# Optimization experiments

Measured on AMD Instinct MI355X. Metric: run time of the kernel, lower is better.

Reference implementation:

```python
import jax, jax.numpy as jnp
import numpy as np

N = 32768          # tokens
D_IN = 1024        # input_dim
H = 512            # hidden_dim
K = 4096           # codebook_size
NC = 3             # num_codebooks


def setup_inputs() -> dict:
    key = jax.random.key(0)
    ks = jax.random.split(key, 7)
    s = 0.02  # small init for linear weights
    return {
        "x": jax.random.normal(ks[0], (N, D_IN), dtype=jnp.float32),
        "enc_w1": jax.random.normal(ks[1], (D_IN, 2 * H), dtype=jnp.float32) * s,
        "enc_b1": jnp.zeros((2 * H,), dtype=jnp.float32),
        "enc_w2": jax.random.normal(ks[2], (2 * H, H), dtype=jnp.float32) * s,
        "enc_b2": jnp.zeros((H,), dtype=jnp.float32),
        "dec_w1": jax.random.normal(ks[3], (H, 2 * H), dtype=jnp.float32) * s,
        "dec_b1": jnp.zeros((2 * H,), dtype=jnp.float32),
        "dec_w2": jax.random.normal(ks[4], (2 * H, D_IN), dtype=jnp.float32) * s,
        "dec_b2": jnp.zeros((D_IN,), dtype=jnp.float32),
        "codebooks": jax.random.normal(ks[5], (NC, K, H), dtype=jnp.float32),
    }


def reference(x, enc_w1, enc_b1, enc_w2, enc_b2,
              dec_w1, dec_b1, dec_w2, dec_b2, codebooks):
    # encoder MLP: [N, D_IN] -> [N, H]
    h = jax.nn.relu(x @ enc_w1 + enc_b1) @ enc_w2 + enc_b2

    residual = h
    quantized = jnp.zeros_like(h)
    indices = []
    for i in range(NC):  # fixed small number of codebook stages
        cb = codebooks[i]  # [K, H]
        # squared Euclidean distances (argmin-equivalent to torch.cdist)
        d = (jnp.sum(residual * residual, axis=1, keepdims=True)
             - 2.0 * residual @ cb.T
             + jnp.sum(cb * cb, axis=1))  # [N, K]
        idx = jnp.argmin(d, axis=1)       # [N]
        sel = cb[idx]                     # gather [N, H]
        indices.append(idx)
        quantized = quantized + sel
        residual = residual - sel

    # decoder MLP: [N, H] -> [N, D_IN]
    reconstructed = jax.nn.relu(quantized @ dec_w1 + dec_b1) @ dec_w2 + dec_b2
    # eval-mode forward: loss is None in the original; omit it here
    return quantized, jnp.stack(indices), reconstructed
```

## Files before the change

kernel.cpp:

```cpp
#include <hip/hip_runtime.h>

#define N_TOK 32768
#define DIN   1024
#define HID   512
#define H2    1024
#define KCB   4096
#define NCB   3
#define CHUNK_E 4096
#define CHUNK_D 8192
#define MARGIN 0.25f

typedef _Float16 f16x8 __attribute__((ext_vector_type(8)));
typedef float f32x4 __attribute__((ext_vector_type(4)));
typedef unsigned short u16;

__device__ inline u16 f2h_bits(float v) {
  union { _Float16 f; u16 u; } cv;
  cv.f = (_Float16)v;
  return cv.u;
}
__device__ inline float h_bits2f(u16 u) {
  union { _Float16 f; u16 u; } cv;
  cv.u = u;
  return (float)cv.f;
}
__device__ inline void fsplit(float v, u16& hi, u16& lo) {
  _Float16 h = (_Float16)v;
  float hf = (float)h;
  union { _Float16 f; u16 u; } ch; ch.f = h; hi = ch.u;
  lo = f2h_bits((v - hf) * 2048.0f);
}

#define SWZ(r) (((r) >> 1) & 3)

__device__ inline void stage16(const u16* gplane, int growbase, int lrowbase,
                               int k0, u16* ldsbase, int l, int stride) {
  const int rp = l >> 2, s = l & 3;
  const int sp = s ^ SWZ(lrowbase + rp);
  const u16* src = gplane + (size_t)(growbase + rp) * stride + k0 + sp * 8;
  __builtin_amdgcn_global_load_lds(
      (const __attribute__((address_space(1))) void*)src,
      (__attribute__((address_space(3))) void*)ldsbase, 16, 0, 0);
}

template <bool RELU, bool SPLIT>
__global__ __launch_bounds__(256) void gemm_f32ek(
    const float* __restrict__ A, const float* __restrict__ B,
    const float* __restrict__ bias, float* __restrict__ C,
    u16* __restrict__ Chi, u16* __restrict__ Clo,
    int M, int K, int Nn) {
  __shared__ float As[16][68];
  __shared__ float Bs[16][68];
  const int tid = threadIdx.x;
  const int tx = tid & 15, ty = tid >> 4;
  const int tx4 = tx * 4, ty4 = ty * 4;
  const int m0 = blockIdx.y * 64, n0 = blockIdx.x * 64;

  const int ar = tid >> 2;
  const int aq = (tid & 3) * 4;
  const int bk = tid >> 4;
  const int bn = (tid & 15) * 4;

  float acc[4][4] = {};

  for (int k0 = 0; k0 < K; k0 += 16) {
    float4 av = *(const float4*)(A + (size_t)(m0 + ar) * K + k0 + aq);
    As[aq + 0][ar] = av.x; As[aq + 1][ar] = av.y;
    As[aq + 2][ar] = av.z; As[aq + 3][ar] = av.w;
    *(float4*)(&Bs[bk][bn]) = *(const float4*)(B + (size_t)(k0 + bk) * Nn + n0 + bn);
    __syncthreads();
#pragma unroll
    for (int kk = 0; kk < 16; ++kk) {
      float4 a4 = *(float4*)(&As[kk][ty4]);
      float4 b4 = *(float4*)(&Bs[kk][tx4]);
      float a[4] = {a4.x, a4.y, a4.z, a4.w};
      float bv[4] = {b4.x, b4.y, b4.z, b4.w};
#pragma unroll
      for (int i = 0; i < 4; ++i)
#pragma unroll
        for (int j = 0; j < 4; ++j) acc[i][j] = fmaf(a[i], bv[j], acc[i][j]);
    }
    __syncthreads();
  }

  float bb[4];
#pragma unroll
  for (int j = 0; j < 4; ++j) bb[j] = bias[n0 + tx4 + j];
#pragma unroll
  for (int i = 0; i < 4; ++i) {
    const size_t row = (size_t)(m0 + ty4 + i);
    if (SPLIT) {
      ushort4 h4, l4;
      u16 hs[4], ls[4];
#pragma unroll
      for (int j = 0; j < 4; ++j) {
        float v = acc[i][j] + bb[j];
        if (RELU) v = v > 0.0f ? v : 0.0f;
        fsplit(v, hs[j], ls[j]);
      }
      h4.x = hs[0]; h4.y = hs[1]; h4.z = hs[2]; h4.w = hs[3];
      l4.x = ls[0]; l4.y = ls[1]; l4.z = ls[2]; l4.w = ls[3];
      *(ushort4*)(&Chi[row * Nn + n0 + tx4]) = h4;
      *(ushort4*)(&Clo[row * Nn + n0 + tx4]) = l4;
    } else {
      float4 o;
      float vv[4];
#pragma unroll
      for (int j = 0; j < 4; ++j) {
        float v = acc[i][j] + bb[j];
        if (RELU) v = v > 0.0f ? v : 0.0f;
        vv[j] = v;
      }
      o.x = vv[0]; o.y = vv[1]; o.z = vv[2]; o.w = vv[3];
      *(float4*)(&C[row * Nn + n0 + tx4]) = o;
    }
  }
}

template <bool RELU, bool F16OUT>
__global__ __launch_bounds__(256) void gemm_mfma_f16(
    const u16* __restrict__ Ahi, const u16* __restrict__ BThi,
    const float* __restrict__ bias,
    float* __restrict__ C, u16* __restrict__ Chi,
    int M, int K, int Nn) {
  __shared__ __attribute__((aligned(16))) u16 As[64 * 32];
  __shared__ __attribute__((aligned(16))) u16 Bs[128 * 32];
  const int tid = threadIdx.x;
  const int w = tid >> 6, l = tid & 63;
  const int wr = w >> 1, wc = w & 1;
  const int lr = l & 15, g = l >> 4;
  const int m0 = blockIdx.y * 64, n0 = blockIdx.x * 128;

  f32x4 acc[2][4];
#pragma unroll
  for (int mr = 0; mr < 2; ++mr)
#pragma unroll
    for (int nr = 0; nr < 4; ++nr) acc[mr][nr] = (f32x4)0.0f;

  for (int ks = 0; ks < K / 32; ++ks) {
    const int k0 = ks * 32;
    __syncthreads();
    stage16(Ahi, m0 + w * 16, w * 16, k0, As + w * 16 * 32, l, K);
    stage16(BThi, n0 + w * 16, w * 16, k0, Bs + w * 16 * 32, l, K);
    stage16(BThi, n0 + (w + 4) * 16, (w + 4) * 16, k0, Bs + (w + 4) * 16 * 32, l, K);
    __syncthreads();

    f16x8 ah[2], bh[4];
#pragma unroll
    for (int mr = 0; mr < 2; ++mr) {
      const int ra = wr * 32 + mr * 16 + lr;
      ah[mr] = *(const f16x8*)(As + ra * 32 + (g ^ SWZ(ra)) * 8);
    }
#pragma unroll
    for (int nr = 0; nr < 4; ++nr) {
      const int rb = wc * 64 + nr * 16 + lr;
      bh[nr] = *(const f16x8*)(Bs + rb * 32 + (g ^ SWZ(rb)) * 8);
    }
#pragma unroll
    for (int mr = 0; mr < 2; ++mr)
#pragma unroll
      for (int nr = 0; nr < 4; ++nr)
        acc[mr][nr] = __builtin_amdgcn_mfma_f32_16x16x32_f16(
            ah[mr], bh[nr], acc[mr][nr], 0, 0, 0);
  }

#pragma unroll
  for (int nr = 0; nr < 4; ++nr) {
    const int col = n0 + wc * 64 + nr * 16 + lr;
    const float bb = bias[col];
#pragma unroll
    for (int mr = 0; mr < 2; ++mr) {
#pragma unroll
      for (int q = 0; q < 4; ++q) {
        const int row = m0 + wr * 32 + mr * 16 + g * 4 + q;
        float v = acc[mr][nr][q] + bb;
        if (RELU) v = v > 0.0f ? v : 0.0f;
        if (F16OUT) Chi[(size_t)row * Nn + col] = f2h_bits(v);
        else C[(size_t)row * Nn + col] = v;
      }
    }
  }
}

__global__ __launch_bounds__(256) void wtsplit(
    const float* __restrict__ W, u16* __restrict__ Thi, u16* __restrict__ Tlo,
    int K, int N) {
  __shared__ float tile[32][33];
  const int k0 = blockIdx.y * 32, n0 = blockIdx.x * 32;
  const int c = threadIdx.x & 31, r8 = threadIdx.x >> 5;
#pragma unroll
  for (int p = 0; p < 4; ++p) {
    const int r = r8 + p * 8;
    tile[r][c] = W[(size_t)(k0 + r) * N + n0 + c];
  }
  __syncthreads();
#pragma unroll
  for (int p = 0; p < 4; ++p) {
    const int r = r8 + p * 8;
    float v = tile[c][r];
    u16 hh, ll;
    fsplit(v, hh, ll);
    Thi[(size_t)(n0 + r) * K + k0 + c] = hh;
    Tlo[(size_t)(n0 + r) * K + k0 + c] = ll;
  }
}

__global__ __launch_bounds__(256) void cbsplit_kernel(
    const float* __restrict__ cb, u16* __restrict__ hi) {
  const size_t i4 = (size_t)blockIdx.x * 256 + threadIdx.x;
  float4 v = *(const float4*)(cb + i4 * 4);
  ushort4 h4;
  u16 dummy;
  fsplit(v.x, h4.x, dummy);
  fsplit(v.y, h4.y, dummy);
  fsplit(v.z, h4.z, dummy);
  fsplit(v.w, h4.w, dummy);
  *(ushort4*)(hi + i4 * 4) = h4;
}

__global__ __launch_bounds__(256) void cnorm_kernel(
    const float* __restrict__ cb, double* __restrict__ cn,
    float* __restrict__ cnf) {
  const int w = blockIdx.x * 4 + (threadIdx.x >> 6);
  const int lane = threadIdx.x & 63;
  const float* row = cb + (size_t)w * HID;
  double s = 0.0;
  for (int h = lane; h < HID; h += 64) {
    double v = (double)row[h];
    s += v * v;
  }
#pragma unroll
  for (int off = 32; off > 0; off >>= 1) s += __shfl_down(s, off, 64);
  if (lane == 0) { cn[w] = s; cnf[w] = (float)s; }
}

__global__ __launch_bounds__(256) void rvq_argmin_p1(
    const u16* __restrict__ Ahi, const u16* __restrict__ Bhi,
    const float* __restrict__ cnf, float* __restrict__ cand) {
  __shared__ __attribute__((aligned(16))) u16 As[2][64 * 32];
  __shared__ __attribute__((aligned(16))) u16 Bs[2][128 * 32];
  __shared__ float4 mt[64][16];

  const int tid = threadIdx.x;
  const int w = tid >> 6, l = tid & 63;
  const int wr = w >> 1, wc = w & 1;
  const int lr = l & 15, g = l >> 4;
  const int bg = (blockIdx.x & 7) * 64 + (blockIdx.x >> 3);
  const int m0 = bg * 64;

  float d0[2][4], d1[2][4];
  int i0[2][4], i1[2][4];
#pragma unroll
  for (int mr = 0; mr < 2; ++mr)
#pragma unroll
    for (int q = 0; q < 4; ++q) {
      d0[mr][q] = 3.4e38f; d1[mr][q] = 3.4e38f;
      i0[mr][q] = 0; i1[mr][q] = 0;
    }

  for (int chunk = 0; chunk < KCB / 128; ++chunk) {
    const int cbase = chunk * 128;
    f32x4 acc[2][4];
#pragma unroll
    for (int mr = 0; mr < 2; ++mr)
#pragma unroll
      for (int nr = 0; nr < 4; ++nr) acc[mr][nr] = (f32x4)0.0f;

    for (int ks8 = 0; ks8 < HID / 64; ++ks8) {
      const int k0 = ks8 * 64;
      __syncthreads();
#pragma unroll
      for (int h = 0; h < 2; ++h) {
        const int kh = k0 + h * 32;
        stage16(Ahi, m0 + w * 16, w * 16, kh, As[h] + w * 16 * 32, l, HID);
        stage16(Bhi, cbase + w * 16, w * 16, kh, Bs[h] + w * 16 * 32, l, HID);
        stage16(Bhi, cbase + (w + 4) * 16, (w + 4) * 16, kh, Bs[h] + (w + 4) * 16 * 32, l, HID);
      }
      __syncthreads();

#pragma unroll 1
      for (int h = 0; h < 2; ++h) {
        f16x8 ah[2], bh[4];
#pragma unroll
        for (int mr = 0; mr < 2; ++mr) {
          const int ra = wr * 32 + mr * 16 + lr;
          ah[mr] = *(const f16x8*)(As[h] + ra * 32 + (g ^ SWZ(ra)) * 8);
        }
#pragma unroll
        for (int nr = 0; nr < 4; ++nr) {
          const int rb = wc * 64 + nr * 16 + lr;
          bh[nr] = *(const f16x8*)(Bs[h] + rb * 32 + (g ^ SWZ(rb)) * 8);
        }
#pragma unroll
        for (int mr = 0; mr < 2; ++mr)
#pragma unroll
          for (int nr = 0; nr < 4; ++nr)
            acc[mr][nr] = __builtin_amdgcn_mfma_f32_16x16x32_f16(
                ah[mr], bh[nr], acc[mr][nr], 0, 0, 0);
      }
    }

#pragma unroll
    for (int nr = 0; nr < 4; ++nr) {
      const int code = cbase + wc * 64 + nr * 16 + lr;
      const float cf = cnf[code];
#pragma unroll
      for (int mr = 0; mr < 2; ++mr) {
#pragma unroll
        for (int q = 0; q < 4; ++q) {
          float d = fmaf(-2.0f, acc[mr][nr][q], cf);
          if (d < d1[mr][q]) {
            if (d < d0[mr][q]) {
              d1[mr][q] = d0[mr][q]; i1[mr][q] = i0[mr][q];
              d0[mr][q] = d; i0[mr][q] = code;
            } else {
              d1[mr][q] = d; i1[mr][q] = code;
            }
          }
        }
      }
    }
  }

  __syncthreads();
  if (wc == 1) {
#pragma unroll
    for (int mr = 0; mr < 2; ++mr)
#pragma unroll
      for (int q = 0; q < 4; ++q) {
        const int tl = wr * 32 + mr * 16 + g * 4 + q;
        float4 e;
        e.x = d0[mr][q]; e.y = (float)i0[mr][q];
        e.z = d1[mr][q]; e.w = (float)i1[mr][q];
        mt[tl][lr] = e;
      }
  }
  __syncthreads();
  if (wc == 0) {
#pragma unroll
    for (int mr = 0; mr < 2; ++mr)
#pragma unroll
      for (int q = 0; q < 4; ++q) {
        const int tl = wr * 32 + mr * 16 + g * 4 + q;
        float4 o = mt[tl][lr];
        float e0d = d0[mr][q], e1d = d1[mr][q];
        int e0i = i0[mr][q], e1i = i1[mr][q];
        int oi0 = (int)o.y, oi1 = (int)o.w;
        if (o.x < e1d) {
          if (o.x < e0d) { e1d = e0d; e1i = e0i; e0d = o.x; e0i = oi0; }
          else { e1d = o.x; e1i = oi0; }
        }
        if (o.z < e1d) {
          if (o.z < e0d) { e1d = e0d; e1i = e0i; e0d = o.z; e0i = oi1; }
          else { e1d = o.z; e1i = oi1; }
        }
        float4 out;
        out.x = e0d; out.y = (float)e0i; out.z = e1d; out.w = (float)e1i;
        *(float4*)(cand + ((size_t)(m0 + tl) * 32 + lr * 2) * 2) = out;
      }
  }
}

__global__ __launch_bounds__(256) void rvq_argmin_p2(
    const float* __restrict__ cand,
    const u16* __restrict__ rhi, const u16* __restrict__ rlo,
    const float* __restrict__ cb, const double* __restrict__ cn,
    int* __restrict__ idxbuf, float* __restrict__ idxout) {
  const int tid = threadIdx.x;
  const int wv = tid >> 6, l = tid & 63;
  const int t = blockIdx.x * 4 + wv;

  float ed = 3.4e38f;
  int ei = 0;
  if (l < 32) {
    float2 e = *(const float2*)(cand + ((size_t)t * 32 + l) * 2);
    ed = e.x;
    ei = (int)e.y;
  }
  float dmin = ed;
#pragma unroll
  for (int off = 32; off > 0; off >>= 1)
    dmin = fminf(dmin, __shfl_xor(dmin, off, 64));
  const bool flag = (l < 32) && (ed <= dmin + MARGIN);
  unsigned long long mask = __ballot(flag);

  const ushort4* hp = (const ushort4*)(rhi + (size_t)t * HID + l * 8);
  const ushort4* lp = (const ushort4*)(rlo + (size_t)t * HID + l * 8);
  ushort4 h0 = hp[0], h1 = hp[1], l0 = lp[0], l1 = lp[1];
  float r[8];
  r[0] = h_bits2f(h0.x) + h_bits2f(l0.x) * (1.0f / 2048.0f);
  r[1] = h_bits2f(h0.y) + h_bits2f(l0.y) * (1.0f / 2048.0f);
  r[2] = h_bits2f(h0.z) + h_bits2f(l0.z) * (1.0f / 2048.0f);
  r[3] = h_bits2f(h0.w) + h_bits2f(l0.w) * (1.0f / 2048.0f);
  r[4] = h_bits2f(h1.x) + h_bits2f(l1.x) * (1.0f / 2048.0f);
  r[5] = h_bits2f(h1.y) + h_bits2f(l1.y) * (1.0f / 2048.0f);
  r[6] = h_bits2f(h1.z) + h_bits2f(l1.z) * (1.0f / 2048.0f);
  r[7] = h_bits2f(h1.w) + h_bits2f(l1.w) * (1.0f / 2048.0f);

  double bd = 1e300;
  int bi = 0;
  while (mask) {
    const int src = __builtin_ctzll(mask);
    mask &= mask - 1;
    const int idx = __shfl(ei, src, 64);
    const float4* crow = (const float4*)(cb + (size_t)idx * HID + l * 8);
    float4 c0 = crow[0], c1 = crow[1];
    double s = (double)r[0] * (double)c0.x + (double)r[1] * (double)c0.y
             + (double)r[2] * (double)c0.z + (double)r[3] * (double)c0.w
             + (double)r[4] * (double)c1.x + (double)r[5] * (double)c1.y
             + (double)r[6] * (double)c1.z + (double)r[7] * (double)c1.w;
#pragma unroll
    for (int off = 32; off > 0; off >>= 1) s += __shfl_xor(s, off, 64);
    const double d = cn[idx] - 2.0 * s;
    if (d < bd || (d == bd && idx < bi)) { bd = d; bi = idx; }
  }
  if (l == 0) {
    idxbuf[t] = bi;
    idxout[t] = (float)bi;
  }
}

template <bool FIRST, bool LAST>
__global__ __launch_bounds__(256) void rvq_update(
    const float* __restrict__ cb, const int* __restrict__ idxbuf,
    float* __restrict__ quant, u16* __restrict__ rhi, u16* __restrict__ rlo) {
  const size_t gid = (size_t)blockIdx.x * blockDim.x + threadIdx.x;
  const int t = (int)(gid >> 7);
  const int q4 = (int)(gid & 127);
  const int idx = idxbuf[t];
  const float4 c = *((const float4*)(cb + (size_t)idx * HID) + q4);
  float4* qp = (float4*)(quant + (size_t)t * HID) + q4;
  float cc[4] = {c.x, c.y, c.z, c.w};
  float qn[4];
  if (FIRST) {
    qn[0] = cc[0]; qn[1] = cc[1]; qn[2] = cc[2]; qn[3] = cc[3];
  } else {
    float4 qv = *qp;
    qn[0] = qv.x + cc[0]; qn[1] = qv.y + cc[1];
    qn[2] = qv.z + cc[2]; qn[3] = qv.w + cc[3];
  }
  ushort4* hp = (ushort4*)(rhi + (size_t)t * HID) + q4;
  ushort4* lp = (ushort4*)(rlo + (size_t)t * HID) + q4;
  ushort4 h4 = *hp, l4 = *lp;
  u16 hs[4] = {h4.x, h4.y, h4.z, h4.w}, ls[4] = {l4.x, l4.y, l4.z, l4.w};
#pragma unroll
  for (int j = 0; j < 4; ++j) {
    if (LAST) {
      fsplit(qn[j], hs[j], ls[j]);
    } else {
      float r = h_bits2f(hs[j]) + h_bits2f(ls[j]) * (1.0f / 2048.0f) - cc[j];
      fsplit(r, hs[j], ls[j]);
    }
  }
  float4 qo;
  qo.x = qn[0]; qo.y = qn[1]; qo.z = qn[2]; qo.w = qn[3];
  *qp = qo;
  h4.x = hs[0]; h4.y = hs[1]; h4.z = hs[2]; h4.w = hs[3];
  l4.x = ls[0]; l4.y = ls[1]; l4.z = ls[2]; l4.w = ls[3];
  *hp = h4;
  *lp = l4;
}

extern "C" void kernel_launch(void* const* d_in, const int* in_sizes, int n_in,
                              void* d_out, int out_size, void* d_ws, size_t ws_size,
                              hipStream_t stream) {
  const float* x      = (const float*)d_in[0];
  const float* enc_w1 = (const float*)d_in[1];
  const float* enc_b1 = (const float*)d_in[2];
  const float* enc_w2 = (const float*)d_in[3];
  const float* enc_b2 = (const float*)d_in[4];
  const float* dec_w1 = (const float*)d_in[5];
  const float* dec_b1 = (const float*)d_in[6];
  const float* dec_w2 = (const float*)d_in[7];
  const float* dec_b2 = (const float*)d_in[8];
  const float* cbs    = (const float*)d_in[9];

  float* quant  = (float*)d_out;
  float* idxout = quant + (size_t)N_TOK * HID;
  float* recon  = idxout + (size_t)NCB * N_TOK;

  char* wsp = (char*)d_ws;
  u16* rhi = (u16*)wsp;       wsp += (size_t)N_TOK * HID * 2;
  u16* rlo = (u16*)wsp;       wsp += (size_t)N_TOK * HID * 2;
  u16* whi = (u16*)wsp;       wsp += (size_t)2560 * 1024 * 2;
  u16* wlo = (u16*)wsp;       wsp += (size_t)2560 * 1024 * 2;
  char* h1region = wsp;       wsp += (size_t)CHUNK_E * H2 * 4;
  int* idxbuf = (int*)wsp;    wsp += (size_t)NCB * N_TOK * 4;
  double* cn = (double*)wsp;  wsp += (size_t)NCB * KCB * 8;
  float* cnf = (float*)wsp;   wsp += (size_t)NCB * KCB * 4;

  u16* dw1Thi = whi;              u16* dw1Tlo = wlo;
  u16* dw2Thi = whi + 524288;     u16* dw2Tlo = wlo + 524288;

  float* h1f  = (float*)h1region;
  u16*   h1hi = (u16*)h1region;
  u16*   cbshi = (u16*)h1region;
  float* cand = (float*)(h1region + (size_t)KCB * HID * 2);

  wtsplit<<<dim3(H2 / 32, HID / 32), 256, 0, stream>>>(dec_w1, dw1Thi, dw1Tlo, HID, H2);
  wtsplit<<<dim3(DIN / 32, H2 / 32), 256, 0, stream>>>(dec_w2, dw2Thi, dw2Tlo, H2, DIN);
  cnorm_kernel<<<NCB * KCB / 4, 256, 0, stream>>>(cbs, cn, cnf);

  for (int c = 0; c < N_TOK / CHUNK_E; ++c) {
    gemm_f32ek<true, false><<<dim3(H2 / 64, CHUNK_E / 64), 256, 0, stream>>>(
        x + (size_t)c * CHUNK_E * DIN, enc_w1, enc_b1, h1f, nullptr, nullptr,
        CHUNK_E, DIN, H2);
    gemm_f32ek<false, true><<<dim3(HID / 64, CHUNK_E / 64), 256, 0, stream>>>(
        h1f, enc_w2, enc_b2, nullptr,
        rhi + (size_t)c * CHUNK_E * HID, rlo + (size_t)c * CHUNK_E * HID,
        CHUNK_E, H2, HID);
  }

  for (int s = 0; s < NCB; ++s) {
    const float* cb = cbs + (size_t)s * KCB * HID;
    cbsplit_kernel<<<(KCB * HID / 4) / 256, 256, 0, stream>>>(cb, cbshi);
    rvq_argmin_p1<<<N_TOK / 64, 256, 0, stream>>>(
        rhi, cbshi, cnf + (size_t)s * KCB, cand);
    rvq_argmin_p2<<<N_TOK / 4, 256, 0, stream>>>(
        cand, rhi, rlo, cb, cn + (size_t)s * KCB,
        idxbuf + (size_t)s * N_TOK, idxout + (size_t)s * N_TOK);
    if (s == 0)
      rvq_update<true, false><<<(N_TOK * 128) / 256, 256, 0, stream>>>(
          cb, idxbuf + (size_t)s * N_TOK, quant, rhi, rlo);
    else if (s < NCB - 1)
      rvq_update<false, false><<<(N_TOK * 128) / 256, 256, 0, stream>>>(
          cb, idxbuf + (size_t)s * N_TOK, quant, rhi, rlo);
    else
      rvq_update<false, true><<<(N_TOK * 128) / 256, 256, 0, stream>>>(
          cb, idxbuf + (size_t)s * N_TOK, quant, rhi, rlo);
  }

  for (int c = 0; c < N_TOK / CHUNK_D; ++c) {
    gemm_mfma_f16<true, true><<<dim3(H2 / 128, CHUNK_D / 64), 256, 0, stream>>>(
        rhi + (size_t)c * CHUNK_D * HID, dw1Thi, dec_b1,
        nullptr, h1hi, CHUNK_D, HID, H2);
    gemm_mfma_f16<false, false><<<dim3(DIN / 128, CHUNK_D / 64), 256, 0, stream>>>(
        h1hi, dw2Thi, dec_b2,
        recon + (size_t)c * CHUNK_D * DIN, nullptr, CHUNK_D, H2, DIN);
  }
}
```

Measured before the change: 2.669 ms.

## Double-buffer LDS tiles in RVQ argmin kernel to overlap loads with MFMA

Flattens the chunk and k-step loops into one iteration space and adds a second LDS buffer, so the next tile is staged while MFMAs run on the current one. A single barrier with an explicit vmcnt wait now replaces the two __syncthreads per step. This is meant to hide global-to-LDS latency. In exchange LDS use doubles, which may lower occupancy. It also depends on stage16 not writing LDS asynchronously in a way the barrier misses.

```diff
diff --git a/kernel.cpp b/kernel.cpp
--- a/kernel.cpp
+++ b/kernel.cpp
@@ -237,8 +237,8 @@
 __global__ __launch_bounds__(256) void rvq_argmin_p1(
     const u16* __restrict__ Ahi, const u16* __restrict__ Bhi,
     const float* __restrict__ cnf, float* __restrict__ cand) {
-  __shared__ __attribute__((aligned(16))) u16 As[2][64 * 32];
-  __shared__ __attribute__((aligned(16))) u16 Bs[2][128 * 32];
+  __shared__ __attribute__((aligned(16))) u16 As[2][2 * 64 * 32];
+  __shared__ __attribute__((aligned(16))) u16 Bs[2][2 * 128 * 32];
   __shared__ float4 mt[64][16];
 
   const int tid = threadIdx.x;
@@ -258,68 +258,85 @@
       i0[mr][q] = 0; i1[mr][q] = 0;
     }
 
-  for (int chunk = 0; chunk < KCB / 128; ++chunk) {
-    const int cbase = chunk * 128;
-    f32x4 acc[2][4];
-#pragma unroll
-    for (int mr = 0; mr < 2; ++mr)
-#pragma unroll
-      for (int nr = 0; nr < 4; ++nr) acc[mr][nr] = (f32x4)0.0f;
-
-    for (int ks8 = 0; ks8 < HID / 64; ++ks8) {
-      const int k0 = ks8 * 64;
-      __syncthreads();
-#pragma unroll
-      for (int h = 0; h < 2; ++h) {
-        const int kh = k0 + h * 32;
-        stage16(Ahi, m0 + w * 16, w * 16, kh, As[h] + w * 16 * 32, l, HID);
-        stage16(Bhi, cbase + w * 16, w * 16, kh, Bs[h] + w * 16 * 32, l, HID);
-        stage16(Bhi, cbase + (w + 4) * 16, (w + 4) * 16, kh, Bs[h] + (w + 4) * 16 * 32, l, HID);
-      }
-      __syncthreads();
+  auto STAGE = [&](int buf, int it) {
+    const int cbase = (it >> 3) * 128;
+    const int k0 = (it & 7) * 64;
+#pragma unroll
+    for (int h = 0; h < 2; ++h) {
+      const int kh = k0 + h * 32;
+      stage16(Ahi, m0 + w * 16, w * 16, kh, As[buf] + h * 2048 + w * 16 * 32, l, HID);
+      stage16(Bhi, cbase + w * 16, w * 16, kh, Bs[buf] + h * 4096 + w * 16 * 32, l, HID);
+      stage16(Bhi, cbase + (w + 4) * 16, (w + 4) * 16, kh, Bs[buf] + h * 4096 + (w + 4) * 16 * 32, l, HID);
+    }
+  };
+
+  f32x4 acc[2][4];
+#pragma unroll
+  for (int mr = 0; mr < 2; ++mr)
+#pragma unroll
+    for (int nr = 0; nr < 4; ++nr) acc[mr][nr] = (f32x4)0.0f;
+
+  int cur = 0;
+  STAGE(0, 0);
+  asm volatile("s_waitcnt vmcnt(0)" ::: "memory");
+  __builtin_amdgcn_s_barrier();
+
+  const int NIT = (KCB / 128) * (HID / 64);
+  for (int it = 0; it < NIT; ++it) {
+    if (it + 1 < NIT) STAGE(cur ^ 1, it + 1);
 
 #pragma unroll 1
-      for (int h = 0; h < 2; ++h) {
-        f16x8 ah[2], bh[4];
+    for (int h = 0; h < 2; ++h) {
+      f16x8 ah[2], bh[4];
+#pragma unroll
+      for (int mr = 0; mr < 2; ++mr) {
+        const int ra = wr * 32 + mr * 16 + lr;
+        ah[mr] = *(const f16x8*)(As[cur] + h * 2048 + ra * 32 + (g ^ SWZ(ra)) * 8);
+      }
+#pragma unroll
+      for (int nr = 0; nr < 4; ++nr) {
+        const int rb = wc * 64 + nr * 16 + lr;
+        bh[nr] = *(const f16x8*)(Bs[cur] + h * 4096 + rb * 32 + (g ^ SWZ(rb)) * 8);
+      }
+#pragma unroll
+      for (int mr = 0; mr < 2; ++mr)
+#pragma unroll
+        for (int nr = 0; nr < 4; ++nr)
+          acc[mr][nr] = __builtin_amdgcn_mfma_f32_16x16x32_f16(
+              ah[mr], bh[nr], acc[mr][nr], 0, 0, 0);
+    }
+
+    if ((it & 7) == 7) {
+      const int cbase = (it >> 3) * 128;
+#pragma unroll
+      for (int nr = 0; nr < 4; ++nr) {
+        const int code = cbase + wc * 64 + nr * 16 + lr;
+        const float cf = cnf[code];
 #pragma unroll
         for (int mr = 0; mr < 2; ++mr) {
-          const int ra = wr * 32 + mr * 16 + lr;
-          ah[mr] = *(const f16x8*)(As[h] + ra * 32 + (g ^ SWZ(ra)) * 8);
-        }
-#pragma unroll
-        for (int nr = 0; nr < 4; ++nr) {
-          const int rb = wc * 64 + nr * 16 + lr;
-          bh[nr] = *(const f16x8*)(Bs[h] + rb * 32 + (g ^ SWZ(rb)) * 8);
-        }
-#pragma unroll
-        for (int mr = 0; mr < 2; ++mr)
-#pragma unroll
-          for (int nr = 0; nr < 4; ++nr)
-            acc[mr][nr] = __builtin_amdgcn_mfma_f32_16x16x32_f16(
-                ah[mr], bh[nr], acc[mr][nr], 0, 0, 0);
-      }
-    }
-
-#pragma unroll
-    for (int nr = 0; nr < 4; ++nr) {
-      const int code = cbase + wc * 64 + nr * 16 + lr;
-      const float cf = cnf[code];
-#pragma unroll
-      for (int mr = 0; mr < 2; ++mr) {
-#pragma unroll
-        for (int q = 0; q < 4; ++q) {
-          float d = fmaf(-2.0f, acc[mr][nr][q], cf);
-          if (d < d1[mr][q]) {
-            if (d < d0[mr][q]) {
-              d1[mr][q] = d0[mr][q]; i1[mr][q] = i0[mr][q];
-              d0[mr][q] = d; i0[mr][q] = code;
-            } else {
-              d1[mr][q] = d; i1[mr][q] = code;
+#pragma unroll
+          for (int q = 0; q < 4; ++q) {
+            float d = fmaf(-2.0f, acc[mr][nr][q], cf);
+            if (d < d1[mr][q]) {
+              if (d < d0[mr][q]) {
+                d1[mr][q] = d0[mr][q]; i1[mr][q] = i0[mr][q];
+                d0[mr][q] = d; i0[mr][q] = code;
+              } else {
+                d1[mr][q] = d; i1[mr][q] = code;
+              }
             }
           }
         }
       }
-    }
+#pragma unroll
+      for (int mr = 0; mr < 2; ++mr)
+#pragma unroll
+        for (int nr = 0; nr < 4; ++nr) acc[mr][nr] = (f32x4)0.0f;
+    }
+
+    asm volatile("s_waitcnt vmcnt(0)" ::: "memory");
+    __builtin_amdgcn_s_barrier();
+    cur ^= 1;
   }
 
   __syncthreads();
```

Result: slower. 2.804 ms (+5.1%).
